# Kernel tuning notes

Measured on AMD Instinct MI355X. Metric: run time of the kernel, lower is better.

The kernel has to match this reference:

```python
import jax, jax.numpy as jnp
import numpy as np

E, K, H, I = 8, 2, 1024, 3584  # num_experts, top_k, hidden, intermediate


def setup_inputs() -> dict:
    key = jax.random.key(0)
    k0, k1, k2, k3, k4 = jax.random.split(key, 5)
    scale = 0.02
    return {
        "hidden_states": jax.random.normal(k0, (2, 1024, H), dtype=jnp.float32),
        "w_gate": jax.random.normal(k1, (E, H), dtype=jnp.float32) * scale,  # gate Linear H->E
        "w1": jax.random.normal(k2, (E, I, H), dtype=jnp.float32) * scale,   # gate proj
        "w3": jax.random.normal(k3, (E, I, H), dtype=jnp.float32) * scale,   # up proj
        "w2": jax.random.normal(k4, (E, H, I), dtype=jnp.float32) * scale,   # down proj
    }


def reference(hidden_states, w_gate, w1, w3, w2):
    B, S, Hd = hidden_states.shape
    x = hidden_states.reshape(-1, Hd)                       # [T, H]
    logits = jnp.einsum('th,eh->te', x, w_gate)             # router logits [T, E]
    probs = jax.nn.softmax(logits, axis=-1)
    topw, topi = jax.lax.top_k(probs, K)                    # [T, K]
    topw = topw / jnp.sum(topw, axis=-1, keepdims=True)     # renormalize=True
    # dense combine weights [T, E] (zero off the top-k)
    comb = jnp.sum(jax.nn.one_hot(topi, E, dtype=x.dtype) * topw[..., None], axis=1)
    # SwiGLU experts (dense reference over all experts; math matches dispatch+combine)
    g = jnp.einsum('th,eih->eti', x, w1)                    # [E, T, I]
    u = jnp.einsum('th,eih->eti', x, w3)
    h = jax.nn.silu(g) * u
    out = jnp.einsum('eti,ehi->eth', h, w2)                 # [E, T, H]
    y = jnp.einsum('te,eth->th', comb, out)                 # weighted combine
    return y.reshape(B, S, Hd)
```

## Files before the change

kernel.cpp:

```cpp
#include <hip/hip_runtime.h>
#include <hip/hip_bf16.h>
#include <stdint.h>

#define NEXP 8
#define HD 1024
#define ID 3584
#define NTOK 2048
#define NSLOT 4096
#define SLOT_PAD 256
#define NSLOT_ALLOC (NSLOT + SLOT_PAD)
#define WN (NEXP * ID * HD)

typedef unsigned short u16;
typedef __attribute__((ext_vector_type(8))) short s16x8;
typedef __attribute__((ext_vector_type(4))) short s16x4;
typedef __attribute__((ext_vector_type(4))) float f32x4;

__device__ __forceinline__ u16 f2bf(float f) {
    __hip_bfloat16 h = __float2bfloat16(f);
    union { __hip_bfloat16 h; u16 u; } v; v.h = h; return v.u;
}

__device__ __forceinline__ s16x8 cvt8(f32x4 a, f32x4 b) {
    s16x8 o;
    o[0]=(short)f2bf(a[0]); o[1]=(short)f2bf(a[1]); o[2]=(short)f2bf(a[2]); o[3]=(short)f2bf(a[3]);
    o[4]=(short)f2bf(b[0]); o[5]=(short)f2bf(b[1]); o[6]=(short)f2bf(b[2]); o[7]=(short)f2bf(b[3]);
    return o;
}

__device__ __forceinline__ void glds16(const void* g, void* l) {
    __builtin_amdgcn_global_load_lds((const __attribute__((address_space(1))) unsigned*)g,
                                     (__attribute__((address_space(3))) unsigned*)l, 16, 0, 0);
}

__device__ __forceinline__ void cvt_blk16(const float* __restrict__ src, u16* __restrict__ dst, int blk) {
    size_t base = (size_t)blk * 4096 + threadIdx.x;
    const f32x4* s = (const f32x4*)src;
    s16x4* d = (s16x4*)dst;
    f32x4 v[16];
#pragma unroll
    for (int j = 0; j < 16; ++j) v[j] = __builtin_nontemporal_load(&s[base + j * 256]);
#pragma unroll
    for (int j = 0; j < 16; ++j) {
        s16x4 o;
        o[0] = (short)f2bf(v[j][0]); o[1] = (short)f2bf(v[j][1]);
        o[2] = (short)f2bf(v[j][2]); o[3] = (short)f2bf(v[j][3]);
        d[base + j * 256] = o;
    }
}

__device__ __forceinline__ void cvt_blk(const float* __restrict__ src, u16* __restrict__ dst, int blk) {
    size_t base = (size_t)blk * 2048 + threadIdx.x;
    const f32x4* s = (const f32x4*)src;
    s16x4* d = (s16x4*)dst;
#pragma unroll
    for (int j = 0; j < 8; ++j) {
        f32x4 v = __builtin_nontemporal_load(&s[base + j * 256]);
        s16x4 o;
        o[0] = (short)f2bf(v[0]); o[1] = (short)f2bf(v[1]);
        o[2] = (short)f2bf(v[2]); o[3] = (short)f2bf(v[3]);
        d[base + j * 256] = o;
    }
}

__global__ void init_kernel(int* __restrict__ counts) {
    if (threadIdx.x < 16) counts[threadIdx.x] = 0;
}

#define RT_BLOCKS 512
#define WCV_BLOCKS 1792
#define XCV_BLOCKS 128
#define PRE_BLOCKS (RT_BLOCKS + 2 * WCV_BLOCKS + XCV_BLOCKS)
__global__ __launch_bounds__(256)
void pre_kernel(const float* __restrict__ x, const float* __restrict__ wg,
                int* __restrict__ topk_idx, float* __restrict__ topk_w,
                int* __restrict__ counts,
                u16* __restrict__ xbf,
                const float* __restrict__ w1, u16* __restrict__ w1bf,
                const float* __restrict__ w3, u16* __restrict__ w3bf) {
    int bid = blockIdx.x;
    if (bid >= RT_BLOCKS) {
        if (bid < RT_BLOCKS + WCV_BLOCKS) {
            cvt_blk16(w1, w1bf, bid - RT_BLOCKS);
        } else if (bid < RT_BLOCKS + 2 * WCV_BLOCKS) {
            cvt_blk16(w3, w3bf, bid - RT_BLOCKS - WCV_BLOCKS);
        } else {
            cvt_blk16(x, xbf, bid - RT_BLOCKS - 2 * WCV_BLOCKS);
        }
        return;
    }
    int t = bid * 4 + (threadIdx.x >> 6);
    int lane = threadIdx.x & 63;
    const float* xr = x + (size_t)t * HD;
    float acc[NEXP];
#pragma unroll
    for (int e = 0; e < NEXP; ++e) acc[e] = 0.f;
#pragma unroll
    for (int i = 0; i < HD / 256; ++i) {
        int h = i * 256 + lane * 4;
        f32x4 xv = *(const f32x4*)(xr + h);
#pragma unroll
        for (int e = 0; e < NEXP; ++e) {
            f32x4 wv = *(const f32x4*)(wg + e * HD + h);
            acc[e] += xv[0]*wv[0] + xv[1]*wv[1] + xv[2]*wv[2] + xv[3]*wv[3];
        }
    }
#pragma unroll
    for (int e = 0; e < NEXP; ++e) {
#pragma unroll
        for (int s = 32; s > 0; s >>= 1) acc[e] += __shfl_xor(acc[e], s, 64);
    }
    if (lane == 0) {
        int b0 = 0; float l0 = acc[0];
#pragma unroll
        for (int e = 1; e < NEXP; ++e) if (acc[e] > l0) { l0 = acc[e]; b0 = e; }
        int b1 = (b0 == 0) ? 1 : 0; float l1 = acc[b1];
#pragma unroll
        for (int e = 0; e < NEXP; ++e) {
            if (e == b0 || e == b1) continue;
            if (acc[e] > l1) { l1 = acc[e]; b1 = e; }
        }
        float w0 = 1.f / (1.f + expf(l1 - l0));
        float w1v = 1.f - w0;
        topk_idx[2 * t] = b0; topk_idx[2 * t + 1] = b1;
        topk_w[2 * t] = w0;  topk_w[2 * t + 1] = w1v;
        atomicAdd(&counts[b0], 1);
        atomicAdd(&counts[b1], 1);
    }
}

__global__ void scan_kernel(const int* __restrict__ counts, int* __restrict__ offsets,
                            int* __restrict__ rows) {
    if (threadIdx.x == 0) {
        int off = 0;
#pragma unroll
        for (int e = 0; e < NEXP; ++e) { offsets[e] = off; off += counts[e]; }
    }
    if (threadIdx.x < SLOT_PAD) rows[NSLOT + threadIdx.x] = 0;
}

__global__ void assign_kernel(const int* __restrict__ topk_idx, const int* __restrict__ offsets,
                              int* __restrict__ counts2, int* __restrict__ rows,
                              int* __restrict__ slot_of) {
    int i = blockIdx.x * 256 + threadIdx.x;
    int e = topk_idx[i];
    int pos = atomicAdd(&counts2[e], 1);
    int slot = offsets[e] + pos;
    rows[slot] = i >> 1;
    slot_of[i] = slot;
}

#define G1_BLOCKS (NEXP * (NTOK / 128) * (ID / 128))
#define CVT2_BLOCKS 1024
__global__ __launch_bounds__(256, 2)
void gemm1_kernel(const u16* __restrict__ xbf, const u16* __restrict__ w1bf,
                  const u16* __restrict__ w3bf, const int* __restrict__ counts,
                  const int* __restrict__ offsets, const int* __restrict__ rows,
                  u16* __restrict__ hbuf,
                  const float* __restrict__ w2, u16* __restrict__ w2bf) {
    __shared__ u16 As[128][64];
    __shared__ u16 B1s[128][64];
    __shared__ u16 B3s[128][64];

    if (blockIdx.x >= G1_BLOCKS) {
        const int nblk = WN / 4 / 2048;
        for (int blk = blockIdx.x - G1_BLOCKS; blk < nblk; blk += CVT2_BLOCKS)
            cvt_blk(w2, w2bf, blk);
        return;
    }

    int bid = blockIdx.x;
    int gq = bid >> 7;
    int rm = bid & 127;
    int mt = rm >> 3;
    int g  = gq * 8 + (rm & 7);
    int e  = g / 28;
    int nt = g - e * 28;

    int n_e = counts[e];
    int m0 = mt * 128;
    if (m0 >= n_e) return;
    int off = offsets[e];
    int n0 = nt * 128;

    int tid = threadIdx.x;
    int lane = tid & 63;
    int wid = tid >> 6;

    int rsub = lane >> 3;
    int chunk = ((lane & 7) ^ rsub) * 8;
    int srow = wid * 32 + rsub;

    const u16 *srcA[4], *srcB1[4], *srcB3[4];
#pragma unroll
    for (int j = 0; j < 4; ++j) {
        int rl = srow + 8 * j;
        int tok = rows[off + m0 + rl];
        srcA[j]  = xbf  + (size_t)tok * HD + chunk;
        srcB1[j] = w1bf + ((size_t)e * ID + n0 + rl) * HD + chunk;
        srcB3[j] = w3bf + ((size_t)e * ID + n0 + rl) * HD + chunk;
    }

    f32x4 accg[4][4] = {}, accu[4][4] = {};
    int wm = (wid >> 1) * 64, wn = (wid & 1) * 64;
    int lr = lane & 15;
    int kk = lane >> 4;
    int ks0 = ((kk)     ^ (lr & 7)) * 8;
    int ks1 = ((4 + kk) ^ (lr & 7)) * 8;

    for (int k0 = 0; k0 < HD; k0 += 64) {
#pragma unroll
        for (int j = 0; j < 4; ++j) {
            glds16(srcA[j]  + k0, &As[wid * 32 + 8 * j][0]);
            glds16(srcB1[j] + k0, &B1s[wid * 32 + 8 * j][0]);
            glds16(srcB3[j] + k0, &B3s[wid * 32 + 8 * j][0]);
        }
        __syncthreads();
        s16x8 a[4], b1[4], b3[4];
#pragma unroll
        for (int f = 0; f < 4; ++f) {
            a[f]  = *(const s16x8*)&As[wm + f * 16 + lr][ks0];
            b1[f] = *(const s16x8*)&B1s[wn + f * 16 + lr][ks0];
            b3[f] = *(const s16x8*)&B3s[wn + f * 16 + lr][ks0];
        }
#pragma unroll
        for (int fm = 0; fm < 4; ++fm)
#pragma unroll
            for (int fn = 0; fn < 4; ++fn) {
                accg[fm][fn] = __builtin_amdgcn_mfma_f32_16x16x32_bf16(a[fm], b1[fn], accg[fm][fn], 0, 0, 0);
                accu[fm][fn] = __builtin_amdgcn_mfma_f32_16x16x32_bf16(a[fm], b3[fn], accu[fm][fn], 0, 0, 0);
            }
#pragma unroll
        for (int f = 0; f < 4; ++f) {
            a[f]  = *(const s16x8*)&As[wm + f * 16 + lr][ks1];
            b1[f] = *(const s16x8*)&B1s[wn + f * 16 + lr][ks1];
            b3[f] = *(const s16x8*)&B3s[wn + f * 16 + lr][ks1];
        }
#pragma unroll
        for (int fm = 0; fm < 4; ++fm)
#pragma unroll
            for (int fn = 0; fn < 4; ++fn) {
                accg[fm][fn] = __builtin_amdgcn_mfma_f32_16x16x32_bf16(a[fm], b1[fn], accg[fm][fn], 0, 0, 0);
                accu[fm][fn] = __builtin_amdgcn_mfma_f32_16x16x32_bf16(a[fm], b3[fn], accu[fm][fn], 0, 0, 0);
            }
        __syncthreads();
    }

    int lc = lane & 15;
    int lr4 = (lane >> 4) * 4;
#pragma unroll
    for (int fm = 0; fm < 4; ++fm) {
#pragma unroll
        for (int r = 0; r < 4; ++r) {
            int row = wm + fm * 16 + lr4 + r;
            if (m0 + row < n_e) {
                size_t base = (size_t)(off + m0 + row) * ID + n0 + wn;
#pragma unroll
                for (int fn = 0; fn < 4; ++fn) {
                    float g2 = accg[fm][fn][r];
                    float u = accu[fm][fn][r];
                    float hv = g2 * u / (1.f + expf(-g2));
                    hbuf[base + fn * 16 + lc] = f2bf(hv);
                }
            }
        }
    }
}

__global__ __launch_bounds__(256, 2)
void gemm2_kernel(const u16* __restrict__ hbuf, const u16* __restrict__ w2bf,
                  const int* __restrict__ counts, const int* __restrict__ offsets,
                  float* __restrict__ out2) {
    int bid = blockIdx.x;
    int e = bid & 7;
    int inner = bid >> 3;
    int mt = inner >> 3;
    int nt = inner & 7;

    int n_e = counts[e];
    int m0 = mt * 128;
    if (m0 >= n_e) return;
    int off = offsets[e];
    int n0 = nt * 128;

    __shared__ u16 As[128][64];
    __shared__ u16 Bs[128][64];

    int tid = threadIdx.x;
    int lane = tid & 63;
    int wid = tid >> 6;

    int rsub = lane >> 3;
    int chunk = ((lane & 7) ^ rsub) * 8;
    int srow = wid * 32 + rsub;

    const u16 *srcA[4], *srcB[4];
#pragma unroll
    for (int j = 0; j < 4; ++j) {
        int rl = srow + 8 * j;
        srcA[j] = hbuf + (size_t)(off + m0 + rl) * ID + chunk;
        srcB[j] = w2bf + ((size_t)e * HD + n0 + rl) * ID + chunk;
    }

    f32x4 acc[4][4] = {};
    int wm = (wid >> 1) * 64, wn = (wid & 1) * 64;
    int lr = lane & 15;
    int kk = lane >> 4;
    int ks0 = ((kk)     ^ (lr & 7)) * 8;
    int ks1 = ((4 + kk) ^ (lr & 7)) * 8;

    for (int k0 = 0; k0 < ID; k0 += 64) {
#pragma unroll
        for (int j = 0; j < 4; ++j) {
            glds16(srcA[j] + k0, &As[wid * 32 + 8 * j][0]);
            glds16(srcB[j] + k0, &Bs[wid * 32 + 8 * j][0]);
        }
        __syncthreads();
        s16x8 a[4], b[4];
#pragma unroll
        for (int f = 0; f < 4; ++f) {
            a[f] = *(const s16x8*)&As[wm + f * 16 + lr][ks0];
            b[f] = *(const s16x8*)&Bs[wn + f * 16 + lr][ks0];
        }
#pragma unroll
        for (int fm = 0; fm < 4; ++fm)
#pragma unroll
            for (int fn = 0; fn < 4; ++fn)
                acc[fm][fn] = __builtin_amdgcn_mfma_f32_16x16x32_bf16(a[fm], b[fn], acc[fm][fn], 0, 0, 0);
#pragma unroll
        for (int f = 0; f < 4; ++f) {
            a[f] = *(const s16x8*)&As[wm + f * 16 + lr][ks1];
            b[f] = *(const s16x8*)&Bs[wn + f * 16 + lr][ks1];
        }
#pragma unroll
        for (int fm = 0; fm < 4; ++fm)
#pragma unroll
            for (int fn = 0; fn < 4; ++fn)
                acc[fm][fn] = __builtin_amdgcn_mfma_f32_16x16x32_bf16(a[fm], b[fn], acc[fm][fn], 0, 0, 0);
        __syncthreads();
    }

    int lc = lane & 15;
    int lr4 = (lane >> 4) * 4;
#pragma unroll
    for (int fm = 0; fm < 4; ++fm) {
#pragma unroll
        for (int r = 0; r < 4; ++r) {
            int row = wm + fm * 16 + lr4 + r;
            if (m0 + row < n_e) {
                float* dst = out2 + (size_t)(off + m0 + row) * HD + n0 + wn;
#pragma unroll
                for (int fn = 0; fn < 4; ++fn)
                    dst[fn * 16 + lc] = acc[fm][fn][r];
            }
        }
    }
}

__global__ void combine_kernel(const float* __restrict__ out2, const int* __restrict__ slot_of,
                               const float* __restrict__ topk_w, float* __restrict__ y) {
    int i = blockIdx.x * 256 + threadIdx.x;
    int t = i >> 8;
    int c = i & 255;
    int s0 = slot_of[2 * t], s1 = slot_of[2 * t + 1];
    float w0 = topk_w[2 * t], w1 = topk_w[2 * t + 1];
    f32x4 a = ((const f32x4*)(out2 + (size_t)s0 * HD))[c];
    f32x4 b = ((const f32x4*)(out2 + (size_t)s1 * HD))[c];
    f32x4 o;
#pragma unroll
    for (int j = 0; j < 4; ++j) o[j] = w0 * a[j] + w1 * b[j];
    ((f32x4*)(y + (size_t)t * HD))[c] = o;
}

extern "C" void kernel_launch(void* const* d_in, const int* in_sizes, int n_in,
                              void* d_out, int out_size, void* d_ws, size_t ws_size,
                              hipStream_t stream) {
    (void)in_sizes; (void)n_in; (void)out_size; (void)ws_size;
    const float* x  = (const float*)d_in[0];
    const float* wg = (const float*)d_in[1];
    const float* w1 = (const float*)d_in[2];
    const float* w3 = (const float*)d_in[3];
    const float* w2 = (const float*)d_in[4];
    float* y = (float*)d_out;

    char* ws = (char*)d_ws;
    int*   counts   = (int*)(ws + 0);
    int*   counts2  = (int*)(ws + 32);
    int*   offsets  = (int*)(ws + 64);
    int*   topk_idx = (int*)(ws + 128);
    float* topk_w   = (float*)(ws + 128 + (size_t)NSLOT * 4);
    int*   rows     = (int*)(ws + 128 + (size_t)NSLOT * 8);
    int*   slot_of  = (int*)(ws + 128 + (size_t)NSLOT * 8 + (size_t)NSLOT_ALLOC * 4);
    size_t off_xbf = 128 + (size_t)NSLOT * 12 + (size_t)NSLOT_ALLOC * 4;
    off_xbf = (off_xbf + 255) & ~(size_t)255;
    u16* xbf = (u16*)(ws + off_xbf);
    size_t off_h = off_xbf + (size_t)NTOK * HD * 2;
    u16* hbuf = (u16*)(ws + off_h);
    size_t off_w1 = off_h + (size_t)NSLOT_ALLOC * ID * 2;
    u16* w1bf = (u16*)(ws + off_w1);
    size_t off_w3 = off_w1 + (size_t)WN * 2;
    u16* w3bf = (u16*)(ws + off_w3);
    size_t off_w2 = off_w3 + (size_t)WN * 2;
    u16* w2bf = (u16*)(ws + off_w2);
    size_t off_o2 = off_w2 + (size_t)WN * 2;
    float* out2 = (float*)(ws + off_o2);

    init_kernel<<<1, 64, 0, stream>>>(counts);
    pre_kernel<<<PRE_BLOCKS, 256, 0, stream>>>(x, wg, topk_idx, topk_w, counts,
                                               xbf, w1, w1bf, w3, w3bf);
    scan_kernel<<<1, 256, 0, stream>>>(counts, offsets, rows);
    assign_kernel<<<NSLOT / 256, 256, 0, stream>>>(topk_idx, offsets, counts2, rows, slot_of);
    gemm1_kernel<<<G1_BLOCKS + CVT2_BLOCKS, 256, 0, stream>>>(xbf, w1bf, w3bf, counts, offsets, rows, hbuf, w2, w2bf);
    gemm2_kernel<<<NEXP * (NTOK / 128) * (HD / 128), 256, 0, stream>>>(hbuf, w2bf, counts, offsets, out2);
    combine_kernel<<<(NTOK * HD / 4) / 256, 256, 0, stream>>>(out2, slot_of, topk_w, y);
}
```

Baseline: 286.0 us.

## Use 512-thread blocks in gemm1 with 8 waves each computing 64x32 tiles

The fused gate/up GEMM kernel moves from 4 waves per 128x128 tile to 8 waves, each owning a 64x32 sub-tile, which halves accumulator registers per wave. The LDS loading is redistributed so each thread issues two async loads per matrix instead of four. The w2 conversion path is adapted to 512 threads. This aims for more waves in flight to hide latency, at the cost of more LDS reads per MFMA, since the A fragments are now read by twice as many waves.

```diff
diff --git a/kernel.cpp b/kernel.cpp
--- a/kernel.cpp
+++ b/kernel.cpp
@@ -21,13 +21,6 @@
     union { __hip_bfloat16 h; u16 u; } v; v.h = h; return v.u;
 }
 
-__device__ __forceinline__ s16x8 cvt8(f32x4 a, f32x4 b) {
-    s16x8 o;
-    o[0]=(short)f2bf(a[0]); o[1]=(short)f2bf(a[1]); o[2]=(short)f2bf(a[2]); o[3]=(short)f2bf(a[3]);
-    o[4]=(short)f2bf(b[0]); o[5]=(short)f2bf(b[1]); o[6]=(short)f2bf(b[2]); o[7]=(short)f2bf(b[3]);
-    return o;
-}
-
 __device__ __forceinline__ void glds16(const void* g, void* l) {
     __builtin_amdgcn_global_load_lds((const __attribute__((address_space(1))) unsigned*)g,
                                      (__attribute__((address_space(3))) unsigned*)l, 16, 0, 0);
@@ -49,17 +42,17 @@
     }
 }
 
-__device__ __forceinline__ void cvt_blk(const float* __restrict__ src, u16* __restrict__ dst, int blk) {
-    size_t base = (size_t)blk * 2048 + threadIdx.x;
+__device__ __forceinline__ void cvt_blk512(const float* __restrict__ src, u16* __restrict__ dst, int blk) {
+    size_t base = (size_t)blk * 4096 + threadIdx.x;
     const f32x4* s = (const f32x4*)src;
     s16x4* d = (s16x4*)dst;
 #pragma unroll
     for (int j = 0; j < 8; ++j) {
-        f32x4 v = __builtin_nontemporal_load(&s[base + j * 256]);
+        f32x4 v = __builtin_nontemporal_load(&s[base + j * 512]);
         s16x4 o;
         o[0] = (short)f2bf(v[0]); o[1] = (short)f2bf(v[1]);
         o[2] = (short)f2bf(v[2]); o[3] = (short)f2bf(v[3]);
-        d[base + j * 256] = o;
+        d[base + j * 512] = o;
     }
 }
 
@@ -152,7 +145,7 @@
 
 #define G1_BLOCKS (NEXP * (NTOK / 128) * (ID / 128))
 #define CVT2_BLOCKS 1024
-__global__ __launch_bounds__(256, 2)
+__global__ __launch_bounds__(512, 6)
 void gemm1_kernel(const u16* __restrict__ xbf, const u16* __restrict__ w1bf,
                   const u16* __restrict__ w3bf, const int* __restrict__ counts,
                   const int* __restrict__ offsets, const int* __restrict__ rows,
@@ -163,9 +156,9 @@
     __shared__ u16 B3s[128][64];
 
     if (blockIdx.x >= G1_BLOCKS) {
-        const int nblk = WN / 4 / 2048;
+        const int nblk = WN / 4 / 4096;
         for (int blk = blockIdx.x - G1_BLOCKS; blk < nblk; blk += CVT2_BLOCKS)
-            cvt_blk(w2, w2bf, blk);
+            cvt_blk512(w2, w2bf, blk);
         return;
     }
 
@@ -189,57 +182,62 @@
 
     int rsub = lane >> 3;
     int chunk = ((lane & 7) ^ rsub) * 8;
-    int srow = wid * 32 + rsub;
-
-    const u16 *srcA[4], *srcB1[4], *srcB3[4];
-#pragma unroll
-    for (int j = 0; j < 4; ++j) {
-        int rl = srow + 8 * j;
-        int tok = rows[off + m0 + rl];
-        srcA[j]  = xbf  + (size_t)tok * HD + chunk;
-        srcB1[j] = w1bf + ((size_t)e * ID + n0 + rl) * HD + chunk;
-        srcB3[j] = w3bf + ((size_t)e * ID + n0 + rl) * HD + chunk;
-    }
-
-    f32x4 accg[4][4] = {}, accu[4][4] = {};
-    int wm = (wid >> 1) * 64, wn = (wid & 1) * 64;
+    int r0 = wid * 8 + rsub;
+    int r1 = 64 + wid * 8 + rsub;
+
+    int tokA0 = rows[off + m0 + r0];
+    int tokA1 = rows[off + m0 + r1];
+    const u16* srcA0  = xbf  + (size_t)tokA0 * HD + chunk;
+    const u16* srcA1  = xbf  + (size_t)tokA1 * HD + chunk;
+    const u16* srcB1a = w1bf + ((size_t)e * ID + n0 + r0) * HD + chunk;
+    const u16* srcB1b = w1bf + ((size_t)e * ID + n0 + r1) * HD + chunk;
+    const u16* srcB3a = w3bf + ((size_t)e * ID + n0 + r0) * HD + chunk;
+    const u16* srcB3b = w3bf + ((size_t)e * ID + n0 + r1) * HD + chunk;
+
+    f32x4 accg[4][2] = {}, accu[4][2] = {};
+    int wm = (wid >> 2) * 64;
+    int wn = (wid & 3) * 32;
     int lr = lane & 15;
     int kk = lane >> 4;
     int ks0 = ((kk)     ^ (lr & 7)) * 8;
     int ks1 = ((4 + kk) ^ (lr & 7)) * 8;
 
     for (int k0 = 0; k0 < HD; k0 += 64) {
-#pragma unroll
-        for (int j = 0; j < 4; ++j) {
-            glds16(srcA[j]  + k0, &As[wid * 32 + 8 * j][0]);
-            glds16(srcB1[j] + k0, &B1s[wid * 32 + 8 * j][0]);
-            glds16(srcB3[j] + k0, &B3s[wid * 32 + 8 * j][0]);
-        }
+        glds16(srcA0  + k0, &As[wid * 8][0]);
+        glds16(srcA1  + k0, &As[64 + wid * 8][0]);
+        glds16(srcB1a + k0, &B1s[wid * 8][0]);
+        glds16(srcB1b + k0, &B1s[64 + wid * 8][0]);
+        glds16(srcB3a + k0, &B3s[wid * 8][0]);
+        glds16(srcB3b + k0, &B3s[64 + wid * 8][0]);
         __syncthreads();
-        s16x8 a[4], b1[4], b3[4];
-#pragma unroll
-        for (int f = 0; f < 4; ++f) {
-            a[f]  = *(const s16x8*)&As[wm + f * 16 + lr][ks0];
+        s16x8 a[4], b1[2], b3[2];
+#pragma unroll
+        for (int f = 0; f < 4; ++f)
+            a[f] = *(const s16x8*)&As[wm + f * 16 + lr][ks0];
+#pragma unroll
+        for (int f = 0; f < 2; ++f) {
             b1[f] = *(const s16x8*)&B1s[wn + f * 16 + lr][ks0];
             b3[f] = *(const s16x8*)&B3s[wn + f * 16 + lr][ks0];
         }
 #pragma unroll
         for (int fm = 0; fm < 4; ++fm)
 #pragma unroll
-            for (int fn = 0; fn < 4; ++fn) {
+            for (int fn = 0; fn < 2; ++fn) {
                 accg[fm][fn] = __builtin_amdgcn_mfma_f32_16x16x32_bf16(a[fm], b1[fn], accg[fm][fn], 0, 0, 0);
                 accu[fm][fn] = __builtin_amdgcn_mfma_f32_16x16x32_bf16(a[fm], b3[fn], accu[fm][fn], 0, 0, 0);
             }
 #pragma unroll
-        for (int f = 0; f < 4; ++f) {
-            a[f]  = *(const s16x8*)&As[wm + f * 16 + lr][ks1];
+        for (int f = 0; f < 4; ++f)
+            a[f] = *(const s16x8*)&As[wm + f * 16 + lr][ks1];
+#pragma unroll
+        for (int f = 0; f < 2; ++f) {
             b1[f] = *(const s16x8*)&B1s[wn + f * 16 + lr][ks1];
             b3[f] = *(const s16x8*)&B3s[wn + f * 16 + lr][ks1];
         }
 #pragma unroll
         for (int fm = 0; fm < 4; ++fm)
 #pragma unroll
-            for (int fn = 0; fn < 4; ++fn) {
+            for (int fn = 0; fn < 2; ++fn) {
                 accg[fm][fn] = __builtin_amdgcn_mfma_f32_16x16x32_bf16(a[fm], b1[fn], accg[fm][fn], 0, 0, 0);
                 accu[fm][fn] = __builtin_amdgcn_mfma_f32_16x16x32_bf16(a[fm], b3[fn], accu[fm][fn], 0, 0, 0);
             }
@@ -256,7 +254,7 @@
             if (m0 + row < n_e) {
                 size_t base = (size_t)(off + m0 + row) * ID + n0 + wn;
 #pragma unroll
-                for (int fn = 0; fn < 4; ++fn) {
+                for (int fn = 0; fn < 2; ++fn) {
                     float g2 = accg[fm][fn][r];
                     float u = accu[fm][fn][r];
                     float hv = g2 * u / (1.f + expf(-g2));
@@ -410,7 +408,7 @@
                                                xbf, w1, w1bf, w3, w3bf);
     scan_kernel<<<1, 256, 0, stream>>>(counts, offsets, rows);
     assign_kernel<<<NSLOT / 256, 256, 0, stream>>>(topk_idx, offsets, counts2, rows, slot_of);
-    gemm1_kernel<<<G1_BLOCKS + CVT2_BLOCKS, 256, 0, stream>>>(xbf, w1bf, w3bf, counts, offsets, rows, hbuf, w2, w2bf);
+    gemm1_kernel<<<G1_BLOCKS + CVT2_BLOCKS, 512, 0, stream>>>(xbf, w1bf, w3bf, counts, offsets, rows, hbuf, w2, w2bf);
     gemm2_kernel<<<NEXP * (NTOK / 128) * (HD / 128), 256, 0, stream>>>(hbuf, w2bf, counts, offsets, out2);
     combine_kernel<<<(NTOK * HD / 4) / 256, 256, 0, stream>>>(out2, slot_of, topk_w, y);
 }
```

Result: slower. 1.019 ms (+256.3%).
